# Kernel tuning notes

Measured on AMD Instinct MI355X. Metric: run time of the kernel, lower is better.

The kernel has to match this reference:

```python
import jax, jax.numpy as jnp
import numpy as np

CAPS1_N = 32 * 6 * 6   # 1152 primary capsules
CAPS1_D = 8            # primary capsule dim
CAPS2_N = 10           # digit capsules
CAPS2_D = 16           # digit capsule dim
ROUTINGS = 3
BATCH = 512


def squash(x, axis=-1):
    # scale = |x|^2 / (1 + |x|^2); out = scale * x / |x|  (matches torch source exactly)
    sq = jnp.sum(x * x, axis=axis, keepdims=True)
    return (sq / (1.0 + sq)) * x / jnp.sqrt(sq)


def setup_inputs() -> dict:
    key = jax.random.key(0)
    k1, k2 = jax.random.split(key)
    x = jax.random.normal(k1, (BATCH, CAPS1_N, CAPS1_D), dtype=jnp.float32)
    weight = 0.01 * jax.random.normal(k2, (CAPS2_N, CAPS1_N, CAPS2_D, CAPS1_D), dtype=jnp.float32)
    return {"x": x, "weight": weight}


def reference(x, weight):
    # x: [B, N1, D1]; weight: [C2, N1, D2, D1]
    # torch: matmul(weight, x[:,None,:,:,None]).squeeze(-1) -> [B, C2, N1, D2]
    x_hat = jnp.einsum('cndk,bnk->bcnd', weight, x)
    x_hat_det = jax.lax.stop_gradient(x_hat)

    B = x.shape[0]
    b = jnp.zeros((B, CAPS2_N, CAPS1_N), dtype=x_hat.dtype)

    # NOTE: the original module returns `outputs` (computed in the i < routings-1
    # branch with x_hat_detached), NOT the last-iteration `out`. We replicate that.
    outputs = None
    for _ in range(ROUTINGS - 1):
        c = jax.nn.softmax(b, axis=1)                                  # softmax over the 10 digit caps
        outputs = squash(jnp.sum(c[..., None] * x_hat_det, axis=-2, keepdims=True))  # [B, C2, 1, D2]
        b = b + jnp.sum(outputs * x_hat_det, axis=-1)                  # [B, C2, N1]
    # final-iteration `out` (squash with non-detached x_hat) is computed in torch
    # but never returned; it does not affect the output, so it is omitted here.
    return jnp.squeeze(outputs, axis=-2)                               # [B, C2, D2]
```

## Files before the change

### kernel.cpp

```cpp
#include <hip/hip_runtime.h>
#include <math.h>


#define BB   512
#define NN1  1152
#define CD   160
#define XB   (NN1*8)
#define WELEM (10*NN1*16*8)

typedef __attribute__((ext_vector_type(8))) short bf16x8;
typedef __attribute__((ext_vector_type(4))) float f32x4;

#define MFMA32(a, b, c) __builtin_amdgcn_mfma_f32_16x16x32_bf16(a, b, c, 0, 0, 0)
#define ZERO4 ((f32x4){0.f, 0.f, 0.f, 0.f})

__device__ __forceinline__ short f2bf(float f) {
    unsigned u = __builtin_bit_cast(unsigned, f);
    u += 0x7FFFu + ((u >> 16) & 1u);
    return (short)(u >> 16);
}
__device__ __forceinline__ float bf2f(short s) {
    unsigned u = ((unsigned)(unsigned short)s) << 16;
    return __builtin_bit_cast(float, u);
}
__device__ __forceinline__ void cvt_hilo8(f32x4 a, f32x4 b, bf16x8& h, bf16x8& l) {
#pragma unroll
    for (int i = 0; i < 4; ++i) {
        short t = f2bf(a[i]); h[i] = t; l[i] = f2bf(a[i] - bf2f(t));
        t = f2bf(b[i]); h[4 + i] = t; l[4 + i] = f2bf(b[i] - bf2f(t));
    }
}
__device__ __forceinline__ int opaque_zero() {
    int z;
    asm volatile("v_mov_b32 %0, 0" : "=v"(z));
    return z;
}
__device__ __forceinline__ void load_lds16(const short* gp, char* lp) {
    __builtin_amdgcn_global_load_lds(
        (const __attribute__((address_space(1))) void*)gp,
        (__attribute__((address_space(3))) void*)lp, 16, 0, 0);
}

__global__ void p0(const float* __restrict__ w,
                   short* __restrict__ wnh, short* __restrict__ wnl)
{
    int i = blockIdx.x * 256 + threadIdx.x;
    float f = w[i];
    short h = f2bf(f);
    wnh[i] = h;
    wnl[i] = f2bf(f - bf2f(h));
}

template<int NS>
__global__ __launch_bounds__(256, 4) void caps_p1(
    const float* __restrict__ x, const short* __restrict__ wnh, const short* __restrict__ wnl,
    float* __restrict__ P)
{
    constexpr int NT = NN1 / NS;
    constexpr int QPW = NT / 16;
    static_assert(NT % 16 == 0, "balanced quads");
    __shared__ float red[2][2560];

    const int ns = blockIdx.x, bt = blockIdx.y;
    const int tid = threadIdx.x, lane = tid & 63, wv = tid >> 6;
    const int lo = lane & 15, g = lane >> 4;
    const int btile = bt * 16;

    f32x4 acc[10];
#pragma unroll
    for (int c = 0; c < 10; ++c) acc[c] = ZERO4;

#pragma unroll 2
    for (int it = 0; it < QPW; ++it) {
        const int n0 = ns * NT + (wv * QPW + it) * 4;
        const float* px = x + (size_t)(btile + lo) * XB + (size_t)(n0 + g) * 8;
        f32x4 x0 = *(const f32x4*)px;
        f32x4 x1 = *(const f32x4*)(px + 4);
        bf16x8 ah, al;
        cvt_hilo8(x0, x1, ah, al);
#pragma unroll
        for (int c = 0; c < 10; ++c) {
            size_t off = (((size_t)c * NN1 + n0 + g) * 16 + lo) * 8;
            bf16x8 bh = *(const bf16x8*)(wnh + off);
            bf16x8 bl = *(const bf16x8*)(wnl + off);
            acc[c] = MFMA32(ah, bh, acc[c]);
            acc[c] = MFMA32(al, bh, acc[c]);
            acc[c] = MFMA32(ah, bl, acc[c]);
        }
    }

    if (wv == 1 || wv == 3) {
        float* s = red[wv >> 1];
#pragma unroll
        for (int c = 0; c < 10; ++c)
#pragma unroll
            for (int e = 0; e < 4; ++e) s[c * 256 + (g * 4 + e) * 16 + lo] = acc[c][e];
    }
    __syncthreads();
    if (wv == 0) {
#pragma unroll
        for (int c = 0; c < 10; ++c)
#pragma unroll
            for (int e = 0; e < 4; ++e) acc[c][e] += red[0][c * 256 + (g * 4 + e) * 16 + lo];
    } else if (wv == 2) {
#pragma unroll
        for (int c = 0; c < 10; ++c)
#pragma unroll
            for (int e = 0; e < 4; ++e) {
                int idx = c * 256 + (g * 4 + e) * 16 + lo;
                red[1][idx] += acc[c][e];
            }
    }
    __syncthreads();
    if (wv == 0) {
        float* dst = P + (size_t)ns * BB * CD;
#pragma unroll
        for (int c = 0; c < 10; ++c)
#pragma unroll
            for (int e = 0; e < 4; ++e)
                dst[(size_t)(btile + g * 4 + e) * CD + c * 16 + lo] =
                    acc[c][e] + red[1][c * 256 + (g * 4 + e) * 16 + lo];
    }
}

__global__ void reduce_squash(const float* __restrict__ P, float* __restrict__ out,
                              int nsplit, float asq)
{
    int t = blockIdx.x * 256 + threadIdx.x;
    float s = 0.f;
    const float* p = P + t;
    for (int ns = 0; ns < nsplit; ++ns, p += (size_t)BB * CD) s += *p;
    float sq = s * s;
#pragma unroll
    for (int m = 1; m < 16; m <<= 1) sq += __shfl_xor(sq, m, 64);
    float qq = asq * sq;
    float sc = qq / (1.f + qq) / sqrtf(sq);
    out[t] = s * sc;
}

template<int NS>
__global__ __launch_bounds__(256, 2) void caps_p2(
    const float* __restrict__ x,
    const short* __restrict__ wnh, const short* __restrict__ wnl,
    const float* __restrict__ o0, float* __restrict__ P)
{
    constexpr int NT = NN1 / NS;
    constexpr int ITER = NT / 8;
    static_assert(NT % 8 == 0, "8n per stage");

    __shared__ __align__(16) char lds[40960];

    const int ns = blockIdx.x, bt = blockIdx.y;
    const int tid = threadIdx.x, lane = tid & 63, wv = tid >> 6;
    const int lo = lane & 15, g = lane >> 4;
    const int btile = bt * 16;
    const int b = btile + lo;

    const int ap_base = ((g == 1) ? 20480 : 0) + wv * 512 + lo * 16;
    const int opq = opaque_zero();
    const float* po0 = o0 + (size_t)b * CD + g * 4;

    f32x4 acc[10];
#pragma unroll
    for (int c = 0; c < 10; ++c) acc[c] = ZERO4;

    const bf16x8 z8 = {0, 0, 0, 0, 0, 0, 0, 0};

    for (int it = 0; it < ITER; ++it) {
        const int n0 = ns * NT + it * 8;

        __syncthreads();
        {
            const short* gsrc = (wv < 2) ? wnh : wnl;
            char* ldst = lds + ((wv < 2) ? 0 : 20480);
            const int segbase = (wv & 1) * 10;
#pragma unroll
            for (int j = 0; j < 10; ++j) {
                const int s = segbase + j;
                const short* gp = gsrc + ((size_t)((s >> 1) * NN1 + n0 + (s & 1) * 4)) * 128 + lane * 8;
                load_lds16(gp, ldst + s * 1024);
            }
        }
        __syncthreads();

        const int na = n0 + wv * 2;
        const float* px = x + (size_t)b * XB + (size_t)na * 8;
        f32x4 x0a = *(const f32x4*)px,       x0b = *(const f32x4*)(px + 4);
        f32x4 x1a = *(const f32x4*)(px + 8), x1b = *(const f32x4*)(px + 12);

        bf16x8 xh0, xl0, xh1, xl1;
        cvt_hilo8(x0a, x0b, xh0, xl0);
        cvt_hilo8(x1a, x1b, xh1, xl1);

        bf16x8 Bx0, Bx1;
        if (g == 3)      { Bx0 = z8;  Bx1 = z8;  }
        else if (g == 2) { Bx0 = xl0; Bx1 = xl1; }
        else             { Bx0 = xh0; Bx1 = xh1; }

        float L0[10], L1[10];
#pragma unroll
        for (int c = 0; c < 10; ++c) {
            bf16x8 A0 = *(const bf16x8*)(lds + ap_base + c * 2048);
            bf16x8 A1 = *(const bf16x8*)(lds + ap_base + c * 2048 + 256);
            f32x4 y0 = MFMA32(A0, Bx0, ZERO4);
            f32x4 y1 = MFMA32(A1, Bx1, ZERO4);
            f32x4 ov = *(const f32x4*)(po0 + c * 16);
            float lp0 = y0[0]*ov[0] + y0[1]*ov[1] + y0[2]*ov[2] + y0[3]*ov[3];
            float lp1 = y1[0]*ov[0] + y1[1]*ov[1] + y1[2]*ov[2] + y1[3]*ov[3];
            lp0 += __shfl_xor(lp0, 16, 64);
            lp0 += __shfl_xor(lp0, 32, 64);
            lp1 += __shfl_xor(lp1, 16, 64);
            lp1 += __shfl_xor(lp1, 32, 64);
            L0[c] = lp0;
            L1[c] = lp1;
        }

        float d0 = 0.f, d1 = 0.f;
#pragma unroll
        for (int c = 0; c < 10; ++c) {
            L0[c] = __expf(L0[c]); d0 += L0[c];
            L1[c] = __expf(L1[c]); d1 += L1[c];
        }
        float i0 = 1.f / d0, i1 = 1.f / d1;

#pragma unroll
        for (int c = 0; c < 10; ++c) {
            bf16x8 A0 = *(const bf16x8*)(lds + opq + ap_base + c * 2048);
            bf16x8 A1 = *(const bf16x8*)(lds + opq + ap_base + c * 2048 + 256);
            f32x4 y0 = MFMA32(A0, Bx0, ZERO4);
            f32x4 y1 = MFMA32(A1, Bx1, ZERO4);
            float c0f = L0[c] * i0, c1f = L1[c] * i1;
#pragma unroll
            for (int e = 0; e < 4; ++e) acc[c][e] += c0f * y0[e] + c1f * y1[e];
        }
    }

    __syncthreads();
    float* red0 = (float*)lds;
    float* red1 = (float*)(lds + 10240);
    if (wv == 1 || wv == 3) {
        float* s = (wv == 1) ? red0 : red1;
#pragma unroll
        for (int c = 0; c < 10; ++c)
#pragma unroll
            for (int e = 0; e < 4; ++e) s[c * 256 + (g * 4 + e) * 16 + lo] = acc[c][e];
    }
    __syncthreads();
    if (wv == 0) {
#pragma unroll
        for (int c = 0; c < 10; ++c)
#pragma unroll
            for (int e = 0; e < 4; ++e) acc[c][e] += red0[c * 256 + (g * 4 + e) * 16 + lo];
    } else if (wv == 2) {
#pragma unroll
        for (int c = 0; c < 10; ++c)
#pragma unroll
            for (int e = 0; e < 4; ++e) {
                int idx = c * 256 + (g * 4 + e) * 16 + lo;
                red1[idx] += acc[c][e];
            }
    }
    __syncthreads();
    if (wv == 0) {
        float* dst = P + (size_t)ns * BB * CD;
#pragma unroll
        for (int c = 0; c < 10; ++c)
#pragma unroll
            for (int e = 0; e < 4; ++e)
                dst[(size_t)(btile + lo) * CD + c * 16 + g * 4 + e] =
                    acc[c][e] + red1[c * 256 + (g * 4 + e) * 16 + lo];
    }
}

extern "C" void kernel_launch(void* const* d_in, const int* in_sizes, int n_in,
                              void* d_out, int out_size, void* d_ws, size_t ws_size,
                              hipStream_t stream)
{
    (void)in_sizes; (void)n_in; (void)out_size;
    const float* x = (const float*)d_in[0];
    const float* w = (const float*)d_in[1];
    float* out = (float*)d_out;

    char* base = (char*)d_ws;
    short* wnh = (short*)(base);
    short* wnl = (short*)(base + 2949120);
    float* o0  = (float*)(base + 5898240);
    float* P   = (float*)(base + 6225920);
    const size_t fixed = 6225920, slab = (size_t)BB * CD * sizeof(float);

    p0<<<WELEM / 256, 256, 0, stream>>>(w, wnh, wnl);

#define LAUNCH_NS(NS1, NS2)                                                            \
    do {                                                                               \
        caps_p1<NS1><<<dim3(NS1, 32), 256, 0, stream>>>(x, wnh, wnl, P);               \
        reduce_squash<<<320, 256, 0, stream>>>(P, o0, NS1, 0.01f);                     \
        caps_p2<NS2><<<dim3(NS2, 32), 256, 0, stream>>>(x, wnh, wnl, o0, P);           \
        reduce_squash<<<320, 256, 0, stream>>>(P, out, NS2, 1.0f);                     \
    } while (0)

    if      (ws_size >= fixed + slab * 36) LAUNCH_NS(36, 36);
    else if (ws_size >= fixed + slab * 12) LAUNCH_NS(12, 12);
    else                                   LAUNCH_NS(4, 4);
#undef LAUNCH_NS
}
```

Measured before the change: 87.87 us.

## Stage weights through LDS in caps_p1 and split capsules across waves

caps_p1 now stages the hi/lo bf16 weight slices for 8 primary capsules per iteration into LDS with direct global-to-LDS loads. Each wave then owns a subset of the 10 digit capsules over all n, where before each wave handled all capsules over a slice of n. This removes the cross-wave LDS reduction and cuts the per-wave accumulator registers from 10 to 3 vectors. In exchange it adds two block barriers per iteration and makes each wave reload x. caps_p2's launch bounds also go from 2 to 4 blocks per CU, which may force register spills.

```diff
diff --git a/kernel.cpp b/kernel.cpp
--- a/kernel.cpp
+++ b/kernel.cpp
@@ -57,69 +57,72 @@
     float* __restrict__ P)
 {
     constexpr int NT = NN1 / NS;
-    constexpr int QPW = NT / 16;
-    static_assert(NT % 16 == 0, "balanced quads");
-    __shared__ float red[2][2560];
+    constexpr int ITER = NT / 8;
+    static_assert(NT % 8 == 0, "8n per stage");
+    __shared__ __align__(16) char lds[40960];
 
     const int ns = blockIdx.x, bt = blockIdx.y;
     const int tid = threadIdx.x, lane = tid & 63, wv = tid >> 6;
     const int lo = lane & 15, g = lane >> 4;
     const int btile = bt * 16;
 
-    f32x4 acc[10];
-#pragma unroll
-    for (int c = 0; c < 10; ++c) acc[c] = ZERO4;
-
-#pragma unroll 2
-    for (int it = 0; it < QPW; ++it) {
-        const int n0 = ns * NT + (wv * QPW + it) * 4;
-        const float* px = x + (size_t)(btile + lo) * XB + (size_t)(n0 + g) * 8;
-        f32x4 x0 = *(const f32x4*)px;
-        f32x4 x1 = *(const f32x4*)(px + 4);
-        bf16x8 ah, al;
-        cvt_hilo8(x0, x1, ah, al);
-#pragma unroll
-        for (int c = 0; c < 10; ++c) {
-            size_t off = (((size_t)c * NN1 + n0 + g) * 16 + lo) * 8;
-            bf16x8 bh = *(const bf16x8*)(wnh + off);
-            bf16x8 bl = *(const bf16x8*)(wnl + off);
-            acc[c] = MFMA32(ah, bh, acc[c]);
-            acc[c] = MFMA32(al, bh, acc[c]);
-            acc[c] = MFMA32(ah, bl, acc[c]);
-        }
-    }
-
-    if (wv == 1 || wv == 3) {
-        float* s = red[wv >> 1];
-#pragma unroll
-        for (int c = 0; c < 10; ++c)
-#pragma unroll
-            for (int e = 0; e < 4; ++e) s[c * 256 + (g * 4 + e) * 16 + lo] = acc[c][e];
-    }
-    __syncthreads();
-    if (wv == 0) {
-#pragma unroll
-        for (int c = 0; c < 10; ++c)
-#pragma unroll
-            for (int e = 0; e < 4; ++e) acc[c][e] += red[0][c * 256 + (g * 4 + e) * 16 + lo];
-    } else if (wv == 2) {
-#pragma unroll
-        for (int c = 0; c < 10; ++c)
-#pragma unroll
-            for (int e = 0; e < 4; ++e) {
-                int idx = c * 256 + (g * 4 + e) * 16 + lo;
-                red[1][idx] += acc[c][e];
+    const int c0 = (wv == 0) ? 0 : (wv == 1) ? 3 : (wv == 2) ? 5 : 8;
+    const int nc = (wv & 1) ? 2 : 3;
+
+    f32x4 acc[3];
+#pragma unroll
+    for (int j = 0; j < 3; ++j) acc[j] = ZERO4;
+
+    for (int it = 0; it < ITER; ++it) {
+        const int n0 = ns * NT + it * 8;
+        __syncthreads();
+        {
+            const short* gsrc = (wv < 2) ? wnh : wnl;
+            char* ldst = lds + ((wv < 2) ? 0 : 20480);
+            const int segbase = (wv & 1) * 10;
+#pragma unroll
+            for (int j = 0; j < 10; ++j) {
+                const int s = segbase + j;
+                const short* gp = gsrc + ((size_t)((s >> 1) * NN1 + n0 + (s & 1) * 4)) * 128 + lane * 8;
+                load_lds16(gp, ldst + s * 1024);
             }
-    }
-    __syncthreads();
-    if (wv == 0) {
-        float* dst = P + (size_t)ns * BB * CD;
-#pragma unroll
-        for (int c = 0; c < 10; ++c)
+        }
+        __syncthreads();
+
+        bf16x8 ah[2], al[2];
+#pragma unroll
+        for (int q = 0; q < 2; ++q) {
+            const float* px = x + (size_t)(btile + lo) * XB + (size_t)(n0 + q * 4 + g) * 8;
+            f32x4 x0 = *(const f32x4*)px;
+            f32x4 x1 = *(const f32x4*)(px + 4);
+            cvt_hilo8(x0, x1, ah[q], al[q]);
+        }
+        const int fb = (g * 16 + lo) * 16;
+#pragma unroll
+        for (int j = 0; j < 3; ++j) {
+            if (j < nc) {
+                const int c = c0 + j;
+#pragma unroll
+                for (int q = 0; q < 2; ++q) {
+                    bf16x8 bh = *(const bf16x8*)(lds + (c * 2 + q) * 1024 + fb);
+                    bf16x8 bl = *(const bf16x8*)(lds + 20480 + (c * 2 + q) * 1024 + fb);
+                    acc[j] = MFMA32(ah[q], bh, acc[j]);
+                    acc[j] = MFMA32(al[q], bh, acc[j]);
+                    acc[j] = MFMA32(ah[q], bl, acc[j]);
+                }
+            }
+        }
+    }
+
+    float* dst = P + (size_t)ns * BB * CD;
+#pragma unroll
+    for (int j = 0; j < 3; ++j) {
+        if (j < nc) {
+            const int c = c0 + j;
 #pragma unroll
             for (int e = 0; e < 4; ++e)
-                dst[(size_t)(btile + g * 4 + e) * CD + c * 16 + lo] =
-                    acc[c][e] + red[1][c * 256 + (g * 4 + e) * 16 + lo];
+                dst[(size_t)(btile + g * 4 + e) * CD + c * 16 + lo] = acc[j][e];
+        }
     }
 }
 
@@ -139,7 +142,7 @@
 }
 
 template<int NS>
-__global__ __launch_bounds__(256, 2) void caps_p2(
+__global__ __launch_bounds__(256, 4) void caps_p2(
     const float* __restrict__ x,
     const short* __restrict__ wnh, const short* __restrict__ wnl,
     const float* __restrict__ o0, float* __restrict__ P)
```

After: 130.9 us. 1.49x slower.
